# Kernel optimization log

Hardware: AMD Instinct MI355X
Metric: run time of the kernel (lower is better)

The kernel has to match this reference:

```python
import jax, jax.numpy as jnp
import numpy as np

N, CAT_IN, H, V, T = 256, 1024, 512, 32000, 8


def setup_inputs() -> dict:
    key = jax.random.key(0)
    ks = jax.random.split(key, 9)
    s = 0.05
    return {
        "context": jax.random.normal(ks[0], (N, CAT_IN), jnp.float32),
        "W_merge": jax.random.normal(ks[1], (H, CAT_IN), jnp.float32) * s,
        "b_merge": jax.random.normal(ks[2], (H,), jnp.float32) * s,
        "W_ih": jax.random.normal(ks[3], (4 * H, H), jnp.float32) * s,
        "W_hh": jax.random.normal(ks[4], (4 * H, H), jnp.float32) * s,
        "b_ih": jax.random.normal(ks[5], (4 * H,), jnp.float32) * s,
        "b_hh": jax.random.normal(ks[6], (4 * H,), jnp.float32) * s,
        "W_out": jax.random.normal(ks[7], (V, H), jnp.float32) * s,
        "b_out": jax.random.normal(ks[8], (V,), jnp.float32) * s,
        "max_subtoken_len": T,
    }


def reference(context, W_merge, b_merge, W_ih, W_hh, b_ih, b_hh, W_out, b_out, max_subtoken_len):
    # merge_func_g_emb: [N, CAT_IN] -> [N, H]
    ctx = context @ W_merge.T + b_merge
    # input projection is constant across steps (same context fed every step)
    x_proj = ctx @ W_ih.T + b_ih  # [N, 4H]
    hdim = W_hh.shape[1]

    def step(carry, _):
        h, c = carry
        gates = x_proj + h @ W_hh.T + b_hh  # [N, 4H]
        i, f, g, o = jnp.split(gates, 4, axis=-1)  # PyTorch LSTM gate order i,f,g,o
        i = jax.nn.sigmoid(i)
        f = jax.nn.sigmoid(f)
        g = jnp.tanh(g)
        o = jax.nn.sigmoid(o)
        c = f * c + i * g
        h = o * jnp.tanh(c)
        logits = h @ W_out.T + b_out  # [N, V]
        return (h, c), logits

    h0 = jnp.zeros((context.shape[0], hdim), context.dtype)
    c0 = jnp.zeros_like(h0)
    _, logits = jax.lax.scan(step, (h0, c0), None, length=max_subtoken_len)  # [T, N, V]
    return jnp.transpose(logits, (1, 0, 2))  # [N, T, V]
```

## Files before the change

kernel.cpp:

```cpp
#include <hip/hip_runtime.h>


#define GLOBAL_AS __attribute__((address_space(1)))
#define LDS_AS __attribute__((address_space(3)))

typedef __attribute__((ext_vector_type(8))) short short8;
typedef __attribute__((ext_vector_type(4))) float f32x4;
typedef unsigned long long u64;

constexpr int N_  = 256;
constexpr int CIN = 1024;
constexpr int H_  = 512;
constexpr int G4  = 2048;
constexpr int V_  = 32000;
constexpr int T_  = 8;

__device__ inline short f2bf(float f) {
  union { float f; unsigned u; } v; v.f = f;
  unsigned r = v.u + 0x7fffu + ((v.u >> 16) & 1u);
  return (short)(r >> 16);
}
__device__ inline unsigned pk2(short a, short b) {
  return ((unsigned)(unsigned short)a) | (((unsigned)(unsigned short)b) << 16);
}

__device__ inline void async16(const void* g, void* l) {
  __builtin_amdgcn_global_load_lds((const GLOBAL_AS unsigned*)g,
                                   (LDS_AS unsigned*)l, 16, 0, 0);
}

__device__ inline float sigm(float x) { return 1.0f / (1.0f + __expf(-x)); }
__device__ inline float tanh_fast(float x) {
  x = fminf(15.0f, fmaxf(-15.0f, x));
  float e = __expf(2.0f * x);
  return (e - 1.0f) / (e + 1.0f);
}

__device__ inline void ag_store32(unsigned* p, unsigned v) {
  __hip_atomic_store(p, v, __ATOMIC_RELAXED, __HIP_MEMORY_SCOPE_AGENT);
}
__device__ inline u64 ag_load64(const u64* p) {
  return __hip_atomic_load(p, __ATOMIC_RELAXED, __HIP_MEMORY_SCOPE_AGENT);
}

__device__ inline void pbar(unsigned* cnt) {
  asm volatile("s_waitcnt vmcnt(0)" ::: "memory");
  __syncthreads();
  if (threadIdx.x == 0) {
    unsigned v = __hip_atomic_fetch_add(cnt, 1u, __ATOMIC_RELAXED,
                                        __HIP_MEMORY_SCOPE_AGENT);
    unsigned tgt = (v & ~15u) + 16u;
    while (__hip_atomic_load(cnt, __ATOMIC_RELAXED, __HIP_MEMORY_SCOPE_AGENT) < tgt)
      __builtin_amdgcn_s_sleep(2);
  }
  __syncthreads();
}

__global__ __launch_bounds__(256) void cvt_all(
    const float* __restrict__ s0, short* __restrict__ d0, int c0,
    const float* __restrict__ s1, short* __restrict__ d1, int c1,
    const float* __restrict__ s2, short* __restrict__ d2, int c2,
    const float* __restrict__ s3, short* __restrict__ d3, int c3,
    const float* __restrict__ s4, short* __restrict__ d4, int c4,
    unsigned* __restrict__ bar) {
  int i = blockIdx.x * 256 + threadIdx.x;
  if (blockIdx.x == 0) bar[threadIdx.x] = 0u;
  const float* s; short* d; int k;
  if (i < c0)                          { s = s0; d = d0; k = i; }
  else if (i < c0 + c1)                { s = s1; d = d1; k = i - c0; }
  else if (i < c0 + c1 + c2)           { s = s2; d = d2; k = i - c0 - c1; }
  else if (i < c0 + c1 + c2 + c3)      { s = s3; d = d3; k = i - c0 - c1 - c2; }
  else if (i < c0 + c1 + c2 + c3 + c4) { s = s4; d = d4; k = i - c0 - c1 - c2 - c3; }
  else return;
  float4 v = ((const float4*)s)[k];
  short4 o;
  o.x = f2bf(v.x); o.y = f2bf(v.y); o.z = f2bf(v.z); o.w = f2bf(v.w);
  ((short4*)d)[k] = o;
}

__global__ __launch_bounds__(256, 1) void decoder_core(
    const short* __restrict__ Ctxin,
    const short* __restrict__ Wmrg,
    const float* __restrict__ bmrg,
    const short* __restrict__ Wih,
    const short* __restrict__ Whh,
    const float* __restrict__ bih,
    const float* __restrict__ bhh,
    short* __restrict__ ctxg,
    short* __restrict__ Hall,
    unsigned* __restrict__ bar)
{
  __shared__ alignas(16) short WhhL[128 * H_];
  __shared__ alignas(16) char scratch[32768];

  const int tid   = threadIdx.x;
  const int lane  = tid & 63;
  const int w     = tid >> 6;
  const int rlane = lane & 15;
  const int klane = (lane >> 4) * 8;
  const int qrow  = (lane >> 4) * 4;
  const int j0    = blockIdx.x * 32;
  const int n0    = blockIdx.y * 32;
  unsigned* mybar = bar + blockIdx.y * 32;
  const int swz   = (rlane & 7) << 4;
  const int hrow  = tid >> 3, hseg = tid & 7;

  {
    short* Aw = (short*)scratch + w * 2048;
    short* Bw = Aw + 1024;
    f32x4 m00 = {0,0,0,0}, m01 = {0,0,0,0}, m10 = {0,0,0,0}, m11 = {0,0,0,0};
    const int kb = w * 256;
    for (int i = 0; i < 8; ++i) {
      int kc = kb + i * 32;
#pragma unroll
      for (int p = 0; p < 2; ++p) {
        int cA = p * 64 + lane;
        async16(Ctxin + (size_t)(n0 + (cA >> 2)) * CIN + kc + (cA & 3) * 8,
                Aw + p * 512);
        async16(Wmrg + (size_t)(j0 + (cA >> 2)) * CIN + kc + (cA & 3) * 8,
                Bw + p * 512);
      }
      asm volatile("s_waitcnt vmcnt(0)" ::: "memory");
      __builtin_amdgcn_sched_barrier(0);
      short8 ma0 = *(const short8*)&Aw[rlane * 32 + klane];
      short8 ma1 = *(const short8*)&Aw[(16 + rlane) * 32 + klane];
      short8 mb0 = *(const short8*)&Bw[rlane * 32 + klane];
      short8 mb1 = *(const short8*)&Bw[(16 + rlane) * 32 + klane];
      m00 = __builtin_amdgcn_mfma_f32_16x16x32_bf16(ma0, mb0, m00, 0, 0, 0);
      m01 = __builtin_amdgcn_mfma_f32_16x16x32_bf16(ma0, mb1, m01, 0, 0, 0);
      m10 = __builtin_amdgcn_mfma_f32_16x16x32_bf16(ma1, mb0, m10, 0, 0, 0);
      m11 = __builtin_amdgcn_mfma_f32_16x16x32_bf16(ma1, mb1, m11, 0, 0, 0);
      asm volatile("s_waitcnt lgkmcnt(0)" ::: "memory");
      __builtin_amdgcn_sched_barrier(0);
    }
    __syncthreads();
    float* G = (float*)scratch;
#pragma unroll
    for (int r = 0; r < 4; ++r) {
      G[(w * 32 + qrow + r) * 32 + rlane]           = m00[r];
      G[(w * 32 + qrow + r) * 32 + 16 + rlane]      = m01[r];
      G[(w * 32 + 16 + qrow + r) * 32 + rlane]      = m10[r];
      G[(w * 32 + 16 + qrow + r) * 32 + 16 + rlane] = m11[r];
    }
    __syncthreads();
    int nn = tid >> 3, jq = tid & 7;
    const float4* Gv = (const float4*)scratch;
    float4 p0 = Gv[(0 * 32 + nn) * 8 + jq];
    float4 p1 = Gv[(1 * 32 + nn) * 8 + jq];
    float4 p2 = Gv[(2 * 32 + nn) * 8 + jq];
    float4 p3 = Gv[(3 * 32 + nn) * 8 + jq];
    int jb = j0 + jq * 4;
    short e0 = f2bf(p0.x + p1.x + p2.x + p3.x + bmrg[jb + 0]);
    short e1 = f2bf(p0.y + p1.y + p2.y + p3.y + bmrg[jb + 1]);
    short e2 = f2bf(p0.z + p1.z + p2.z + p3.z + bmrg[jb + 2]);
    short e3 = f2bf(p0.w + p1.w + p2.w + p3.w + bmrg[jb + 3]);
    unsigned* cp = (unsigned*)&ctxg[(size_t)(n0 + nn) * H_ + jb];
    ag_store32(cp + 0, pk2(e0, e1));
    ag_store32(cp + 1, pk2(e2, e3));
  }
  pbar(mybar);

  {
    const u64* rp = (const u64*)(ctxg + (size_t)(n0 + hrow) * H_);
    u64 cv[16];
#pragma unroll
    for (int i = 0; i < 16; ++i)
      cv[i] = ag_load64(rp + i * 8 + hseg);
    char* CL = (char*)WhhL;
#pragma unroll
    for (int i = 0; i < 16; ++i)
      *(u64*)(CL + ((hrow * 1024 + i * 64 + hseg * 8) ^ ((hrow & 7) << 4))) = cv[i];
  }
  __syncthreads();

  f32x4 x00, x01, x10, x11;
  {
    int ng0 = w * H_ + j0 + rlane, ng1 = ng0 + 16;
    float bc0 = bih[ng0] + bhh[ng0];
    float bc1 = bih[ng1] + bhh[ng1];
    x00 = (f32x4){bc0, bc0, bc0, bc0};  x01 = (f32x4){bc1, bc1, bc1, bc1};
    x10 = x00;                          x11 = x01;
    short* Bs = (short*)scratch;
    const char* CLb = (const char*)WhhL;
    for (int kc = 0; kc < H_; kc += 32) {
#pragma unroll
      for (int p = 0; p < 2; ++p) {
        int idx = p * 256 + tid;
        int br = idx >> 2, q = idx & 3;
        async16(Wih + (size_t)((br >> 5) * H_ + j0 + (br & 31)) * H_ + q * 8 + kc,
                &Bs[(idx & ~63) * 8]);
      }
      __syncthreads();
      int ko = (kc + klane) * 2;
      short8 xa0 = *(const short8*)(CLb + ((rlane * 1024 + ko) ^ swz));
      short8 xa1 = *(const short8*)(CLb + (((16 + rlane) * 1024 + ko) ^ swz));
      short8 xb0 = *(const short8*)&Bs[(w * 32 + rlane) * 32 + klane];
      short8 xb1 = *(const short8*)&Bs[(w * 32 + 16 + rlane) * 32 + klane];
      x00 = __builtin_amdgcn_mfma_f32_16x16x32_bf16(xa0, xb0, x00, 0, 0, 0);
      x01 = __builtin_amdgcn_mfma_f32_16x16x32_bf16(xa0, xb1, x01, 0, 0, 0);
      x10 = __builtin_amdgcn_mfma_f32_16x16x32_bf16(xa1, xb0, x10, 0, 0, 0);
      x11 = __builtin_amdgcn_mfma_f32_16x16x32_bf16(xa1, xb1, x11, 0, 0, 0);
      __syncthreads();
    }
  }

#pragma unroll
  for (int i = 0; i < 32; ++i) {
    int c = i * 256 + tid;
    int r = c >> 6, cq = c & 63;
    int ks = ((cq << 4) ^ ((r & 7) << 4)) >> 1;
    async16(Whh + (size_t)((r >> 5) * H_ + j0 + (r & 31)) * H_ + ks,
            &WhhL[(size_t)(i * 256 + (tid & ~63)) * 8]);
  }

  float creg[4] = {0.f, 0.f, 0.f, 0.f};
  const int ne = tid >> 3, jq = tid & 7;
  const int r_b0 = w * 32 + rlane, r_b1 = r_b0 + 16;
  const char* WLb = (const char*)WhhL;
  char* HLb = (char*)scratch;

  for (int t = 0; t < T_; ++t) {
    f32x4 a00 = x00, a01 = x01, a10 = x10, a11 = x11;
    if (t > 0) {
      const short* Hp = Hall + (size_t)(t - 1) * N_ * H_;
      const u64* rp = (const u64*)(Hp + (size_t)(n0 + hrow) * H_);
      u64 hv[16];
#pragma unroll
      for (int i = 0; i < 16; ++i)
        hv[i] = ag_load64(rp + i * 8 + hseg);
#pragma unroll
      for (int i = 0; i < 16; ++i)
        *(u64*)(HLb + ((hrow * 1024 + i * 64 + hseg * 8) ^ ((hrow & 7) << 4))) = hv[i];
      __syncthreads();
#pragma unroll
      for (int kc = 0; kc < H_; kc += 32) {
        int ko = (kc + klane) * 2;
        short8 a0 = *(const short8*)(HLb + ((rlane * 1024 + ko) ^ swz));
        short8 a1 = *(const short8*)(HLb + (((16 + rlane) * 1024 + ko) ^ swz));
        short8 b0 = *(const short8*)(WLb + ((r_b0 * 1024 + ko) ^ swz));
        short8 b1 = *(const short8*)(WLb + ((r_b1 * 1024 + ko) ^ swz));
        a00 = __builtin_amdgcn_mfma_f32_16x16x32_bf16(a0, b0, a00, 0, 0, 0);
        a01 = __builtin_amdgcn_mfma_f32_16x16x32_bf16(a0, b1, a01, 0, 0, 0);
        a10 = __builtin_amdgcn_mfma_f32_16x16x32_bf16(a1, b0, a10, 0, 0, 0);
        a11 = __builtin_amdgcn_mfma_f32_16x16x32_bf16(a1, b1, a11, 0, 0, 0);
      }
      __syncthreads();
    }
    float* G = (float*)scratch;
#pragma unroll
    for (int r = 0; r < 4; ++r) {
      G[(w * 32 + qrow + r) * 32 + rlane]           = a00[r];
      G[(w * 32 + qrow + r) * 32 + 16 + rlane]      = a01[r];
      G[(w * 32 + 16 + qrow + r) * 32 + rlane]      = a10[r];
      G[(w * 32 + 16 + qrow + r) * 32 + 16 + rlane] = a11[r];
    }
    __syncthreads();
    float4 gi = ((const float4*)G)[(0 * 32 + ne) * 8 + jq];
    float4 gf = ((const float4*)G)[(1 * 32 + ne) * 8 + jq];
    float4 gg = ((const float4*)G)[(2 * 32 + ne) * 8 + jq];
    float4 go = ((const float4*)G)[(3 * 32 + ne) * 8 + jq];
    float pi[4] = {gi.x, gi.y, gi.z, gi.w};
    float pf[4] = {gf.x, gf.y, gf.z, gf.w};
    float pg[4] = {gg.x, gg.y, gg.z, gg.w};
    float po[4] = {go.x, go.y, go.z, go.w};
    short hv4[4];
#pragma unroll
    for (int e = 0; e < 4; ++e) {
      float ii = sigm(pi[e]), ff = sigm(pf[e]);
      float g2 = tanh_fast(pg[e]), oo = sigm(po[e]);
      float cv = ff * creg[e] + ii * g2;
      creg[e] = cv;
      hv4[e] = f2bf(oo * tanh_fast(cv));
    }
    unsigned* hp = (unsigned*)&Hall[(size_t)t * N_ * H_
                                    + (size_t)(n0 + ne) * H_ + j0 + jq * 4];
    ag_store32(hp + 0, pk2(hv4[0], hv4[1]));
    ag_store32(hp + 1, pk2(hv4[2], hv4[3]));
    if (t < T_ - 1) pbar(mybar);
  }
}

template<int BM, int BN, int MODE>
__global__ __launch_bounds__(256) void gemm_bf16_bt(
    const short* __restrict__ A, const short* __restrict__ B,
    const float* __restrict__ bias1, const float* __restrict__ bias2,
    void* __restrict__ Cv, int M, int N, int K)
{
  constexpr int RT = BM / 32;
  constexpr int CT = BN / 32;
  __shared__ short As[BM * 32];
  __shared__ short Bs[BN * 32];

  const int tid = threadIdx.x;
  const int lane = tid & 63;
  const int w = tid >> 6;
  const int wr = w >> 1, wc = w & 1;
  const int m0 = blockIdx.y * BM;
  const int n0 = blockIdx.x * BN;
  const int rlane = lane & 15;
  const int klane = (lane >> 4) * 8;

  f32x4 acc[RT][CT] = {};

  for (int kc = 0; kc < K; kc += 32) {
#pragma unroll
    for (int it = 0; it < (BM * 4) / 256; ++it) {
      int idx = it * 256 + tid;
      const short* g = A + (size_t)(m0 + (idx >> 2)) * K + kc + (idx & 3) * 8;
      async16(g, &As[(size_t)(it * 256 + (tid & ~63)) * 8]);
    }
#pragma unroll
    for (int it = 0; it < (BN * 4) / 256; ++it) {
      int idx = it * 256 + tid;
      const short* g = B + (size_t)(n0 + (idx >> 2)) * K + kc + (idx & 3) * 8;
      async16(g, &Bs[(size_t)(it * 256 + (tid & ~63)) * 8]);
    }
    __syncthreads();

    short8 af[RT], bfr[CT];
#pragma unroll
    for (int rt = 0; rt < RT; ++rt)
      af[rt] = *(const short8*)&As[(wr * (RT * 16) + rt * 16 + rlane) * 32 + klane];
#pragma unroll
    for (int ct = 0; ct < CT; ++ct)
      bfr[ct] = *(const short8*)&Bs[(wc * (CT * 16) + ct * 16 + rlane) * 32 + klane];
#pragma unroll
    for (int rt = 0; rt < RT; ++rt)
#pragma unroll
      for (int ct = 0; ct < CT; ++ct)
        acc[rt][ct] = __builtin_amdgcn_mfma_f32_16x16x32_bf16(af[rt], bfr[ct],
                                                              acc[rt][ct], 0, 0, 0);
    __syncthreads();
  }

#pragma unroll
  for (int ct = 0; ct < CT; ++ct) {
    int ng = n0 + wc * (CT * 16) + ct * 16 + rlane;
    float bv = (bias1 ? bias1[ng] : 0.0f) + (bias2 ? bias2[ng] : 0.0f);
#pragma unroll
    for (int rt = 0; rt < RT; ++rt)
#pragma unroll
      for (int r = 0; r < 4; ++r) {
        int mg = m0 + wr * (RT * 16) + rt * 16 + (lane >> 4) * 4 + r;
        float v = acc[rt][ct][r] + bv;
        if (MODE == 2) {
          int t = mg >> 8, nb = mg & 255;
          ((float*)Cv)[(size_t)nb * (T_ * V_) + (size_t)t * V_ + ng] = v;
        } else if (MODE == 1) {
          ((short*)Cv)[(size_t)mg * N + ng] = f2bf(v);
        } else {
          ((float*)Cv)[(size_t)mg * N + ng] = v;
        }
      }
  }
}

extern "C" void kernel_launch(void* const* d_in, const int* in_sizes, int n_in,
                              void* d_out, int out_size, void* d_ws, size_t ws_size,
                              hipStream_t stream)
{
  (void)in_sizes; (void)n_in; (void)out_size; (void)ws_size;
  const float* context = (const float*)d_in[0];
  const float* W_merge = (const float*)d_in[1];
  const float* b_merge = (const float*)d_in[2];
  const float* W_ih    = (const float*)d_in[3];
  const float* W_hh    = (const float*)d_in[4];
  const float* b_ih    = (const float*)d_in[5];
  const float* b_hh    = (const float*)d_in[6];
  const float* W_out   = (const float*)d_in[7];
  const float* b_out   = (const float*)d_in[8];
  float* out = (float*)d_out;

  char* p = (char*)d_ws;
  short* Wout_b  = (short*)p;  p += (size_t)V_ * H_ * 2;
  short* Whh_b   = (short*)p;  p += (size_t)G4 * H_ * 2;
  short* Wih_b   = (short*)p;  p += (size_t)G4 * H_ * 2;
  short* Wmrg_b  = (short*)p;  p += (size_t)H_ * CIN * 2;
  short* Ctxin_b = (short*)p;  p += (size_t)N_ * CIN * 2;
  short* Ctx_b   = (short*)p;  p += (size_t)N_ * H_ * 2;
  short* Hall    = (short*)p;  p += (size_t)T_ * N_ * H_ * 2;
  unsigned* bar  = (unsigned*)p; p += 256 * 4;

  {
    int c0 = V_ * H_ / 4, c1 = N_ * CIN / 4, c2 = H_ * CIN / 4;
    int c3 = G4 * H_ / 4, c4 = G4 * H_ / 4;
    int tot = c0 + c1 + c2 + c3 + c4;
    cvt_all<<<(tot + 255) / 256, 256, 0, stream>>>(
        W_out, Wout_b, c0, context, Ctxin_b, c1, W_merge, Wmrg_b, c2,
        W_ih, Wih_b, c3, W_hh, Whh_b, c4, bar);
  }

  decoder_core<<<dim3(H_ / 32, N_ / 32), 256, 0, stream>>>(
      Ctxin_b, Wmrg_b, b_merge, Wih_b, Whh_b, b_ih, b_hh, Ctx_b, Hall, bar);

  gemm_bf16_bt<128, 128, 2><<<dim3(V_ / 128, (T_ * N_) / 128), 256, 0, stream>>>(
      Hall, Wout_b, b_out, nullptr, out, T_ * N_, V_, H_);
}
```

Baseline: 498.0 us.

## Double-buffer logits GEMM with swizzled LDS, BK=64, and XCD-aware block mapping

Replaces the generic templated GEMM for the output projection with a specialised kernel. It double-buffers LDS tiles with K-chunks of 64, so the next tile's global loads overlap MFMA work on the current one. It XOR-swizzles the LDS layout to avoid bank conflicts and remaps block IDs so neighbouring tiles land on the same XCD for L2 reuse of W_out. It also raises wave priority around the MFMA bursts, which adds LDS usage and hand-placed waitcnt and barrier logic.

```diff
diff --git a/kernel.cpp b/kernel.cpp
--- a/kernel.cpp
+++ b/kernel.cpp
@@ -280,77 +280,102 @@
   }
 }
 
-template<int BM, int BN, int MODE>
-__global__ __launch_bounds__(256) void gemm_bf16_bt(
-    const short* __restrict__ A, const short* __restrict__ B,
-    const float* __restrict__ bias1, const float* __restrict__ bias2,
-    void* __restrict__ Cv, int M, int N, int K)
+__global__ __launch_bounds__(256) void gemm_logits(
+    const short* __restrict__ A,
+    const short* __restrict__ B,
+    const float* __restrict__ bias,
+    float* __restrict__ out)
 {
-  constexpr int RT = BM / 32;
-  constexpr int CT = BN / 32;
-  __shared__ short As[BM * 32];
-  __shared__ short Bs[BN * 32];
-
-  const int tid = threadIdx.x;
-  const int lane = tid & 63;
-  const int w = tid >> 6;
-  const int wr = w >> 1, wc = w & 1;
-  const int m0 = blockIdx.y * BM;
-  const int n0 = blockIdx.x * BN;
+  constexpr int BK = 64;
+  constexpr int NT = H_ / BK;
+  __shared__ alignas(16) short As[2][128 * BK];
+  __shared__ alignas(16) short Bs[2][128 * BK];
+
+  const int tid   = threadIdx.x;
+  const int lane  = tid & 63;
+  const int w     = tid >> 6;
+  const int wr    = w >> 1, wc = w & 1;
   const int rlane = lane & 15;
   const int klane = (lane >> 4) * 8;
 
-  f32x4 acc[RT][CT] = {};
-
-  for (int kc = 0; kc < K; kc += 32) {
-#pragma unroll
-    for (int it = 0; it < (BM * 4) / 256; ++it) {
+  int bid = (int)blockIdx.x;
+  int lid = (bid & 7) * 500 + (bid >> 3);
+  const int m0 = (lid & 15) * 128;
+  const int n0 = (lid >> 4) * 128;
+
+  f32x4 acc[4][4] = {};
+
+  auto stage = [&](int b, int kt) {
+    const int kc = kt * BK;
+#pragma unroll
+    for (int it = 0; it < 4; ++it) {
       int idx = it * 256 + tid;
-      const short* g = A + (size_t)(m0 + (idx >> 2)) * K + kc + (idx & 3) * 8;
-      async16(g, &As[(size_t)(it * 256 + (tid & ~63)) * 8]);
-    }
-#pragma unroll
-    for (int it = 0; it < (BN * 4) / 256; ++it) {
+      int r = idx >> 3, sg = idx & 7;
+      async16(A + (size_t)(m0 + r) * H_ + kc + ((sg ^ (r & 7)) << 3),
+              &As[b][(idx & ~63) * 8]);
+    }
+#pragma unroll
+    for (int it = 0; it < 4; ++it) {
       int idx = it * 256 + tid;
-      const short* g = B + (size_t)(n0 + (idx >> 2)) * K + kc + (idx & 3) * 8;
-      async16(g, &Bs[(size_t)(it * 256 + (tid & ~63)) * 8]);
-    }
-    __syncthreads();
-
-    short8 af[RT], bfr[CT];
-#pragma unroll
-    for (int rt = 0; rt < RT; ++rt)
-      af[rt] = *(const short8*)&As[(wr * (RT * 16) + rt * 16 + rlane) * 32 + klane];
-#pragma unroll
-    for (int ct = 0; ct < CT; ++ct)
-      bfr[ct] = *(const short8*)&Bs[(wc * (CT * 16) + ct * 16 + rlane) * 32 + klane];
-#pragma unroll
-    for (int rt = 0; rt < RT; ++rt)
-#pragma unroll
-      for (int ct = 0; ct < CT; ++ct)
-        acc[rt][ct] = __builtin_amdgcn_mfma_f32_16x16x32_bf16(af[rt], bfr[ct],
-                                                              acc[rt][ct], 0, 0, 0);
-    __syncthreads();
-  }
-
-#pragma unroll
-  for (int ct = 0; ct < CT; ++ct) {
-    int ng = n0 + wc * (CT * 16) + ct * 16 + rlane;
-    float bv = (bias1 ? bias1[ng] : 0.0f) + (bias2 ? bias2[ng] : 0.0f);
-#pragma unroll
-    for (int rt = 0; rt < RT; ++rt)
+      int r = idx >> 3, sg = idx & 7;
+      async16(B + (size_t)(n0 + r) * H_ + kc + ((sg ^ (r & 7)) << 3),
+              &Bs[b][(idx & ~63) * 8]);
+    }
+  };
+
+  stage(0, 0);
+  for (int kt = 0; kt < NT; ++kt) {
+    const int cur = kt & 1;
+    if (kt + 1 < NT) {
+      stage(cur ^ 1, kt + 1);
+      asm volatile("s_waitcnt vmcnt(8)" ::: "memory");
+    } else {
+      asm volatile("s_waitcnt vmcnt(0)" ::: "memory");
+    }
+    __builtin_amdgcn_sched_barrier(0);
+    __builtin_amdgcn_s_barrier();
+    const char* Ab = (const char*)As[cur];
+    const char* Bb = (const char*)Bs[cur];
+#pragma unroll
+    for (int ks = 0; ks < 2; ++ks) {
+      short8 af[4], bf[4];
+#pragma unroll
+      for (int rt = 0; rt < 4; ++rt) {
+        int row = wr * 64 + rt * 16 + rlane;
+        af[rt] = *(const short8*)(Ab +
+            ((row * 128 + ks * 64 + klane * 2) ^ ((row & 7) << 4)));
+      }
+#pragma unroll
+      for (int ct = 0; ct < 4; ++ct) {
+        int row = wc * 64 + ct * 16 + rlane;
+        bf[ct] = *(const short8*)(Bb +
+            ((row * 128 + ks * 64 + klane * 2) ^ ((row & 7) << 4)));
+      }
+      asm volatile("s_waitcnt lgkmcnt(0)" ::: "memory");
+      __builtin_amdgcn_sched_barrier(0);
+      __builtin_amdgcn_s_setprio(1);
+#pragma unroll
+      for (int rt = 0; rt < 4; ++rt)
+#pragma unroll
+        for (int ct = 0; ct < 4; ++ct)
+          acc[rt][ct] = __builtin_amdgcn_mfma_f32_16x16x32_bf16(
+              af[rt], bf[ct], acc[rt][ct], 0, 0, 0);
+      __builtin_amdgcn_s_setprio(0);
+    }
+    __builtin_amdgcn_s_barrier();
+  }
+
+#pragma unroll
+  for (int ct = 0; ct < 4; ++ct) {
+    int ng = n0 + wc * 64 + ct * 16 + rlane;
+    float bv = bias[ng];
+#pragma unroll
+    for (int rt = 0; rt < 4; ++rt)
 #pragma unroll
       for (int r = 0; r < 4; ++r) {
-        int mg = m0 + wr * (RT * 16) + rt * 16 + (lane >> 4) * 4 + r;
-        float v = acc[rt][ct][r] + bv;
-        if (MODE == 2) {
-          int t = mg >> 8, nb = mg & 255;
-          ((float*)Cv)[(size_t)nb * (T_ * V_) + (size_t)t * V_ + ng] = v;
-        } else if (MODE == 1) {
-          ((short*)Cv)[(size_t)mg * N + ng] = f2bf(v);
-        } else {
-          ((float*)Cv)[(size_t)mg * N + ng] = v;
-        }
+        int mg = m0 + wr * 64 + rt * 16 + (lane >> 4) * 4 + r;
+        int t = mg >> 8, nb = mg & 255;
+        out[(size_t)nb * (T_ * V_) + (size_t)t * V_ + ng] = acc[rt][ct][r] + bv;
       }
   }
 }
@@ -393,6 +418,5 @@
   decoder_core<<<dim3(H_ / 32, N_ / 32), 256, 0, stream>>>(
       Ctxin_b, Wmrg_b, b_merge, Wih_b, Whh_b, b_ih, b_hh, Ctx_b, Hall, bar);
 
-  gemm_bf16_bt<128, 128, 2><<<dim3(V_ / 128, (T_ * N_) / 128), 256, 0, stream>>>(
-      Hall, Wout_b, b_out, nullptr, out, T_ * N_, V_, H_);
-}
+  gemm_logits<<<dim3(4000), 256, 0, stream>>>(Hall, Wout_b, b_out, out);
+}
```

New measurement: 459.0 us. -7.8%, faster.
